# Kernel optimization log

Measured on AMD Instinct MI355X. Metric: run time of the kernel, lower is better.

Reference implementation:

```python
import jax, jax.numpy as jnp
from jax import lax
import numpy as np

DIM = 64
EMB = 48
PATCH = 8


def setup_inputs() -> dict:
    key = jax.random.key(0)
    ks = jax.random.split(key, 8)
    b, H, W = 4, 256, 256
    x = jax.random.normal(ks[0], (b, DIM, H, W), dtype=jnp.float32)
    prior = jax.random.normal(ks[1], (b, 1, EMB * 4), dtype=jnp.float32)
    # nn.Linear(embed_dim*4, dim*2, bias=False): weight [out, in]
    w_kernel = jax.random.normal(ks[2], (DIM * 2, EMB * 4), dtype=jnp.float32) * 0.05
    # Conv2d(dim, dim*6, 1)
    w_hidden = jax.random.normal(ks[3], (DIM * 6, DIM, 1, 1), dtype=jnp.float32) * 0.05
    # Conv2d(dim*6, dim*6, 3, padding=1, groups=dim*3) -> OIHW with I = 6*dim/(3*dim) = 2
    w_dw = jax.random.normal(ks[4], (DIM * 6, 2, 3, 3), dtype=jnp.float32) * 0.05
    # Conv2d(dim*2, dim, 1)
    w_proj = jax.random.normal(ks[5], (DIM, DIM * 2, 1, 1), dtype=jnp.float32) * 0.05
    ln_weight = jnp.ones((DIM * 2,), dtype=jnp.float32)
    ln_bias = jnp.zeros((DIM * 2,), dtype=jnp.float32)
    return {"x": x, "prior": prior, "w_kernel": w_kernel, "w_hidden": w_hidden,
            "w_dw": w_dw, "w_proj": w_proj, "ln_weight": ln_weight, "ln_bias": ln_bias}


def _patchify(t):
    # b c (h p1) (w p2) -> b c h w p1 p2
    b, c, H, W = t.shape
    t = t.reshape(b, c, H // PATCH, PATCH, W // PATCH, PATCH)
    return t.transpose(0, 1, 2, 4, 3, 5)


def _unpatchify(t):
    # b c h w p1 p2 -> b c (h p1) (w p2)
    b, c, h, w, p1, p2 = t.shape
    return t.transpose(0, 1, 2, 4, 3, 5).reshape(b, c, h * p1, w * p2)


def reference(x, prior, w_kernel, w_hidden, w_dw, w_proj, ln_weight, ln_bias):
    # prior modulation (group == 1 path)
    kv = jnp.einsum('blf,kf->blk', prior, w_kernel)[:, 0]  # [b, 2*dim]
    kv1 = kv[:, :DIM, None, None]
    kv2 = kv[:, DIM:, None, None]
    x = x * kv1 + kv2

    # 1x1 conv to hidden (6*dim channels)
    hidden = jnp.einsum('bchw,oc->bohw', x, w_hidden[:, :, 0, 0])

    # depthwise-ish 3x3 grouped conv, groups = 3*dim
    qkv = lax.conv_general_dilated(
        hidden, w_dw, window_strides=(1, 1), padding='SAME',
        feature_group_count=3 * DIM,
        dimension_numbers=('NCHW', 'OIHW', 'NCHW'))
    q, k, v = jnp.split(qkv, 3, axis=1)  # each [b, 2*dim, H, W]

    # frequency-domain correlation on 8x8 patches
    q_f = jnp.fft.rfft2(_patchify(q))
    k_f = jnp.fft.rfft2(_patchify(k))
    out = jnp.fft.irfft2(q_f * k_f, s=(PATCH, PATCH))
    out = _unpatchify(out)

    # WithBias LayerNorm over channel dim (to_3d puts channels last)
    mu = jnp.mean(out, axis=1, keepdims=True)
    var = jnp.mean((out - mu) ** 2, axis=1, keepdims=True)
    out = (out - mu) / jnp.sqrt(var + 1e-5)
    out = out * ln_weight[None, :, None, None] + ln_bias[None, :, None, None]

    # gate with v and project out
    output = v * out
    output = jnp.einsum('bchw,oc->bohw', output, w_proj[:, :, 0, 0])
    return output
```

## Files before the change

### kernel.cpp

```cpp
#include <hip/hip_runtime.h>


#define HW    65536
#define SLAB  64
#define HROWS 66
#define HSZ2  (HROWS*256)
#define QS    16384

__device__ __forceinline__ unsigned short f2bf(float f) {
    unsigned u = __float_as_uint(f);
    u += 0x7FFFu + ((u >> 16) & 1u);
    return (unsigned short)(u >> 16);
}
__device__ __forceinline__ float bflo(unsigned u) { return __uint_as_float(u << 16); }
__device__ __forceinline__ float bfhi(unsigned u) { return __uint_as_float(u & 0xFFFF0000u); }

__global__ void k_prep(const float* __restrict__ prior, const float* __restrict__ wk,
                       const float* __restrict__ wh, const float* __restrict__ wp,
                       float* __restrict__ kv, float* __restrict__ whT, float* __restrict__ wpT) {
    int t = blockIdx.x * 256 + threadIdx.x;
    if (t < 512) {
        int b = t >> 7, k = t & 127;
        const float* p = prior + b * 192;
        const float* w = wk + k * 192;
        float s = 0.f;
        for (int f = 0; f < 192; ++f) s = fmaf(p[f], w[f], s);
        kv[t] = s;
        return;
    }
    t -= 512;
    if (t < 24576) {
        int c = t / 384, o = t - c * 384;
        whT[t] = wh[o * 64 + c];
        return;
    }
    t -= 24576;
    int c = t >> 6, o = t & 63;
    wpT[t] = wp[o * 128 + c];
}

__global__ __launch_bounds__(256, 4) void k2_hidden(const float* __restrict__ x,
    const float* __restrict__ whT, const float* __restrict__ kv,
    unsigned short* __restrict__ hid, int r0) {
    int row = blockIdx.x * 2 + (threadIdx.x >> 7);
    int cp = threadIdx.x & 127;
    int chunk = blockIdx.y;
    int b = blockIdx.z;
    int g = r0 - 1 + row;
    unsigned* hb = (unsigned*)(hid + ((size_t)(b * 384 + chunk * 32)) * HSZ2
                               + row * 256 + cp * 2);
    if (g < 0 || g > 255) {
        #pragma unroll
        for (int j = 0; j < 32; ++j) hb[(size_t)j * (HSZ2 / 2)] = 0u;
        return;
    }
    const float2* xb = (const float2*)(x + (size_t)b * 64 * HW + g * 256 + cp * 2);
    const float* kv1 = kv + b * 128;
    const float* kv2 = kv1 + 64;
    float acc0[32], acc1[32];
    #pragma unroll
    for (int j = 0; j < 32; ++j) { acc0[j] = 0.f; acc1[j] = 0.f; }
    #pragma unroll 4
    for (int c = 0; c < 64; ++c) {
        float2 xv = xb[(size_t)c * (HW / 2)];
        float xp0 = fmaf(xv.x, kv1[c], kv2[c]);
        float xp1 = fmaf(xv.y, kv1[c], kv2[c]);
        const float* wr = whT + c * 384 + chunk * 32;
        #pragma unroll
        for (int j = 0; j < 32; ++j) {
            acc0[j] = fmaf(wr[j], xp0, acc0[j]);
            acc1[j] = fmaf(wr[j], xp1, acc1[j]);
        }
    }
    #pragma unroll
    for (int j = 0; j < 32; ++j)
        hb[(size_t)j * (HSZ2 / 2)] = (unsigned)f2bf(acc0[j]) | ((unsigned)f2bf(acc1[j]) << 16);
}

__global__ __launch_bounds__(256) void k3_dw(const unsigned short* __restrict__ hid,
    const float* __restrict__ wdw, unsigned short* __restrict__ qkv) {
    __shared__ float sIn[2 * 18 * 66];
    int t = threadIdx.x;
    int bid = blockIdx.x;
    int gl = blockIdx.y;
    int b = blockIdx.z;
    int tx = bid & 3, ty = bid >> 2;
    int x0 = tx * 64, y0 = ty * 16;
    const unsigned short* hbase = hid + ((size_t)(b * 384 + 2 * gl)) * HSZ2;
    for (int idx = t; idx < 2 * 18 * 66; idx += 256) {
        int chl = idx >= 1188;
        int rem = idx - chl * 1188;
        int row = rem / 66;
        int col = rem - row * 66;
        int gx = x0 + col - 1;
        float v = 0.f;
        if (gx >= 0 && gx < 256)
            v = bflo((unsigned)hbase[(size_t)chl * HSZ2 + (y0 + row) * 256 + gx]);
        sIn[idx] = v;
    }
    __syncthreads();
    int og = 2 * gl;
    float w0[18], w1[18];
    #pragma unroll
    for (int i = 0; i < 18; ++i) {
        w0[i] = wdw[(size_t)og * 18 + i];
        w1[i] = wdw[(size_t)(og + 1) * 18 + i];
    }
    unsigned short* q0 = qkv + ((size_t)(b * 384 + og)) * QS;
    #pragma unroll
    for (int pp = 0; pp < 2; ++pp) {
        int ly = pp * 8 + (t >> 5);
        int lxp = (t & 31) * 2;
        float a[2][2];
        #pragma unroll
        for (int px = 0; px < 2; ++px) {
            float s0 = 0.f, s1 = 0.f;
            #pragma unroll
            for (int i = 0; i < 2; ++i)
                #pragma unroll
                for (int ky = 0; ky < 3; ++ky)
                    #pragma unroll
                    for (int kx = 0; kx < 3; ++kx) {
                        float v = sIn[i * 1188 + (ly + ky) * 66 + (lxp + px + kx)];
                        s0 = fmaf(w0[i * 9 + ky * 3 + kx], v, s0);
                        s1 = fmaf(w1[i * 9 + ky * 3 + kx], v, s1);
                    }
            a[px][0] = s0; a[px][1] = s1;
        }
        int row = y0 + ly;
        int gx = x0 + lxp;
        int patch = (row >> 3) * 32 + (gx >> 3);
        int off = patch * 64 + (row & 7) * 8 + (gx & 7);
        ((unsigned*)(q0 + off))[0] =
            (unsigned)f2bf(a[0][0]) | ((unsigned)f2bf(a[1][0]) << 16);
        ((unsigned*)(q0 + QS + off))[0] =
            (unsigned)f2bf(a[0][1]) | ((unsigned)f2bf(a[1][1]) << 16);
    }
}

__global__ __launch_bounds__(256, 2) void kC_patch(const unsigned short* __restrict__ qkv,
    const float* __restrict__ wpT, const float* __restrict__ lnw,
    const float* __restrict__ lnb, float* __restrict__ outp, int r0) {
    __shared__ __align__(16) float sBuf[128 * 68];
    __shared__ __align__(16) float sMu[64];
    __shared__ __align__(16) float sRstd[64];
    int t = threadIdx.x;
    int p = blockIdx.x;
    int b = blockIdx.y;
    int c = t & 127;
    int pyh = t >> 7;

    const uint4* gq = (const uint4*)(qkv + ((size_t)(b * 384 + c)) * QS + p * 64);
    const uint4* gk = (const uint4*)(qkv + ((size_t)(b * 384 + 128 + c)) * QS + p * 64);
    float q[64], k[64];
    #pragma unroll
    for (int f = 0; f < 8; ++f) {
        uint4 u = gq[f];
        q[f * 8 + 0] = bflo(u.x); q[f * 8 + 1] = bfhi(u.x);
        q[f * 8 + 2] = bflo(u.y); q[f * 8 + 3] = bfhi(u.y);
        q[f * 8 + 4] = bflo(u.z); q[f * 8 + 5] = bfhi(u.z);
        q[f * 8 + 6] = bflo(u.w); q[f * 8 + 7] = bfhi(u.w);
    }
    #pragma unroll
    for (int s = 0; s < 8; ++s) {
        int r = (s + 4 * pyh) & 7;
        uint4 u = ((const uint4*)gk)[r];
        k[s * 8 + 0] = bflo(u.x); k[s * 8 + 1] = bfhi(u.x);
        k[s * 8 + 2] = bflo(u.y); k[s * 8 + 3] = bfhi(u.y);
        k[s * 8 + 4] = bflo(u.z); k[s * 8 + 5] = bfhi(u.z);
        k[s * 8 + 6] = bflo(u.w); k[s * 8 + 7] = bfhi(u.w);
    }
    float acc[4][8];
    #pragma unroll
    for (int it = 0; it < 4; ++it)
        #pragma unroll
        for (int px = 0; px < 8; ++px) acc[it][px] = 0.f;
    #pragma unroll
    for (int iy = 0; iy < 8; ++iy)
        #pragma unroll
        for (int ix = 0; ix < 8; ++ix) {
            float qv = q[iy * 8 + ix];
            #pragma unroll
            for (int it = 0; it < 4; ++it) {
                int ks = (it - iy) & 7;
                #pragma unroll
                for (int px = 0; px < 8; ++px)
                    acc[it][px] = fmaf(qv, k[ks * 8 + ((px - ix) & 7)], acc[it][px]);
            }
        }
    #pragma unroll
    for (int it = 0; it < 4; ++it) {
        int pix0 = pyh * 32 + it * 8;
        *(float4*)&sBuf[c * 68 + pix0] =
            make_float4(acc[it][0], acc[it][1], acc[it][2], acc[it][3]);
        *(float4*)&sBuf[c * 68 + pix0 + 4] =
            make_float4(acc[it][4], acc[it][5], acc[it][6], acc[it][7]);
    }
    const uint4* gv = (const uint4*)(qkv + ((size_t)(b * 384 + 256 + c)) * QS
                                     + p * 64 + pyh * 32);
    float vv[32];
    #pragma unroll
    for (int f = 0; f < 4; ++f) {
        uint4 u = gv[f];
        vv[f * 8 + 0] = bflo(u.x); vv[f * 8 + 1] = bfhi(u.x);
        vv[f * 8 + 2] = bflo(u.y); vv[f * 8 + 3] = bfhi(u.y);
        vv[f * 8 + 4] = bflo(u.z); vv[f * 8 + 5] = bfhi(u.z);
        vv[f * 8 + 6] = bflo(u.w); vv[f * 8 + 7] = bfhi(u.w);
    }
    float lw = lnw[c], lb = lnb[c];
    __syncthreads();

    {
        int q4 = (t >> 4) & 3;
        int px = (t & 15) | ((t >> 6) << 4);
        float s = 0.f, s2 = 0.f;
        #pragma unroll
        for (int j = 0; j < 32; ++j) {
            float v = sBuf[(q4 * 32 + j) * 68 + px];
            s += v;
            s2 = fmaf(v, v, s2);
        }
        s  += __shfl_xor(s, 16);   s2 += __shfl_xor(s2, 16);
        s  += __shfl_xor(s, 32);   s2 += __shfl_xor(s2, 32);
        if ((t & 48) == 0) {
            float mu = s * (1.f / 128.f);
            float var = s2 * (1.f / 128.f) - mu * mu;
            sMu[px] = mu;
            sRstd[px] = rsqrtf(var + 1e-5f);
        }
    }
    __syncthreads();
    #pragma unroll
    for (int it = 0; it < 4; ++it) {
        int pix0 = pyh * 32 + it * 8;
        float4 ma = *(const float4*)&sMu[pix0];
        float4 mb = *(const float4*)&sMu[pix0 + 4];
        float4 ra = *(const float4*)&sRstd[pix0];
        float4 rb = *(const float4*)&sRstd[pix0 + 4];
        float mus[8] = {ma.x, ma.y, ma.z, ma.w, mb.x, mb.y, mb.z, mb.w};
        float rss[8] = {ra.x, ra.y, ra.z, ra.w, rb.x, rb.y, rb.z, rb.w};
        #pragma unroll
        for (int px = 0; px < 8; ++px) {
            float tv = fmaf((acc[it][px] - mus[px]) * rss[px], lw, lb)
                       * vv[it * 8 + px];
            sBuf[(pix0 + px) * 132 + c] = tv;
        }
    }
    __syncthreads();
    {
        int px = t & 63;
        int og = __builtin_amdgcn_readfirstlane((t >> 6) * 16);
        float po[16];
        #pragma unroll
        for (int j = 0; j < 16; ++j) po[j] = 0.f;
        const float4* tb = (const float4*)&sBuf[px * 132];
        #pragma unroll 4
        for (int k4 = 0; k4 < 32; ++k4) {
            float4 tv = tb[k4];
            const float* w0 = wpT + (k4 * 4 + 0) * 64 + og;
            const float* w1 = wpT + (k4 * 4 + 1) * 64 + og;
            const float* w2 = wpT + (k4 * 4 + 2) * 64 + og;
            const float* w3 = wpT + (k4 * 4 + 3) * 64 + og;
            #pragma unroll
            for (int j = 0; j < 16; ++j)
                po[j] = fmaf(w0[j], tv.x,
                        fmaf(w1[j], tv.y,
                        fmaf(w2[j], tv.z,
                        fmaf(w3[j], tv.w, po[j]))));
        }
        int grow = r0 + (p >> 5) * 8 + (px >> 3);
        int gcol = (p & 31) * 8 + (px & 7);
        float* ob = outp + ((size_t)(b * 64 + og)) * HW + grow * 256 + gcol;
        #pragma unroll
        for (int j = 0; j < 16; ++j) ob[(size_t)j * HW] = po[j];
    }
}

extern "C" void kernel_launch(void* const* d_in, const int* in_sizes, int n_in,
                              void* d_out, int out_size, void* d_ws, size_t ws_size,
                              hipStream_t stream) {
    const float* x     = (const float*)d_in[0];
    const float* prior = (const float*)d_in[1];
    const float* wk    = (const float*)d_in[2];
    const float* wh    = (const float*)d_in[3];
    const float* wdw   = (const float*)d_in[4];
    const float* wp    = (const float*)d_in[5];
    const float* lnw   = (const float*)d_in[6];
    const float* lnb   = (const float*)d_in[7];
    float* out = (float*)d_out;
    float* ws  = (float*)d_ws;

    float* kv  = ws;
    float* whT = ws + 512;
    float* wpT = ws + 512 + 24576;
    unsigned short* hid = (unsigned short*)(ws + 40960);
    unsigned short* qkv = hid + (size_t)4 * 384 * HSZ2;

    k_prep<<<dim3(130), dim3(256), 0, stream>>>(prior, wk, wh, wp, kv, whT, wpT);
    for (int slab = 0; slab < 4; ++slab) {
        int r0 = slab * SLAB;
        k2_hidden<<<dim3(HROWS / 2, 12, 4), dim3(256), 0, stream>>>(x, whT, kv, hid, r0);
        k3_dw<<<dim3(16, 192, 4), dim3(256), 0, stream>>>(hid, wdw, qkv);
        kC_patch<<<dim3(256, 4), dim3(256), 0, stream>>>(qkv, wpT, lnw, lnb, out, r0);
    }
}
```

Before: 683.9 us.

## Restructure hidden 1x1 conv to load x once per pixel and loop output chunks

The hidden-projection kernel now assigns one pixel per thread and 192 output channels per block, instead of two pixels per thread and 32 channels per block. The 64 modulated input channels are loaded once into registers and reused across three 64-channel accumulator passes. This cuts redundant x reads, which before were repeated across 12 channel chunks. The cost is heavy register pressure (64 inputs plus 64 accumulators), a lower occupancy target, fewer blocks, and 16-bit stores instead of packed 32-bit stores.

```diff
diff --git a/kernel.cpp b/kernel.cpp
--- a/kernel.cpp
+++ b/kernel.cpp
@@ -39,42 +39,47 @@
     wpT[t] = wp[o * 128 + c];
 }
 
-__global__ __launch_bounds__(256, 4) void k2_hidden(const float* __restrict__ x,
+__global__ __launch_bounds__(256, 3) void k2_hidden(const float* __restrict__ x,
     const float* __restrict__ whT, const float* __restrict__ kv,
     unsigned short* __restrict__ hid, int r0) {
-    int row = blockIdx.x * 2 + (threadIdx.x >> 7);
-    int cp = threadIdx.x & 127;
-    int chunk = blockIdx.y;
+    int row = blockIdx.x;
+    int px  = threadIdx.x;
+    int half = blockIdx.y;
     int b = blockIdx.z;
     int g = r0 - 1 + row;
-    unsigned* hb = (unsigned*)(hid + ((size_t)(b * 384 + chunk * 32)) * HSZ2
-                               + row * 256 + cp * 2);
+    unsigned short* hb = hid + ((size_t)(b * 384 + half * 192)) * HSZ2
+                         + row * 256 + px;
     if (g < 0 || g > 255) {
-        #pragma unroll
-        for (int j = 0; j < 32; ++j) hb[(size_t)j * (HSZ2 / 2)] = 0u;
+        #pragma unroll 8
+        for (int j = 0; j < 192; ++j) hb[(size_t)j * HSZ2] = 0;
         return;
     }
-    const float2* xb = (const float2*)(x + (size_t)b * 64 * HW + g * 256 + cp * 2);
+    const float* xb = x + (size_t)b * 64 * HW + (size_t)g * 256 + px;
     const float* kv1 = kv + b * 128;
     const float* kv2 = kv1 + 64;
-    float acc0[32], acc1[32];
-    #pragma unroll
-    for (int j = 0; j < 32; ++j) { acc0[j] = 0.f; acc1[j] = 0.f; }
-    #pragma unroll 4
-    for (int c = 0; c < 64; ++c) {
-        float2 xv = xb[(size_t)c * (HW / 2)];
-        float xp0 = fmaf(xv.x, kv1[c], kv2[c]);
-        float xp1 = fmaf(xv.y, kv1[c], kv2[c]);
-        const float* wr = whT + c * 384 + chunk * 32;
-        #pragma unroll
-        for (int j = 0; j < 32; ++j) {
-            acc0[j] = fmaf(wr[j], xp0, acc0[j]);
-            acc1[j] = fmaf(wr[j], xp1, acc1[j]);
-        }
-    }
-    #pragma unroll
-    for (int j = 0; j < 32; ++j)
-        hb[(size_t)j * (HSZ2 / 2)] = (unsigned)f2bf(acc0[j]) | ((unsigned)f2bf(acc1[j]) << 16);
+    float xp[64];
+    #pragma unroll
+    for (int c = 0; c < 64; ++c)
+        xp[c] = fmaf(xb[(size_t)c * HW], kv1[c], kv2[c]);
+    #pragma unroll
+    for (int ch = 0; ch < 3; ++ch) {
+        const float* wbase = whT + half * 192 + ch * 64;
+        float acc[64];
+        #pragma unroll
+        for (int j = 0; j < 64; ++j) acc[j] = 0.f;
+        #pragma unroll 4
+        for (int c = 0; c < 64; ++c) {
+            float xv = xp[c];
+            const float* wr = wbase + c * 384;
+            #pragma unroll
+            for (int j = 0; j < 64; ++j)
+                acc[j] = fmaf(wr[j], xv, acc[j]);
+        }
+        unsigned short* hc = hb + (size_t)(ch * 64) * HSZ2;
+        #pragma unroll
+        for (int j = 0; j < 64; ++j)
+            hc[(size_t)j * HSZ2] = f2bf(acc[j]);
+    }
 }
 
 __global__ __launch_bounds__(256) void k3_dw(const unsigned short* __restrict__ hid,
@@ -299,7 +304,7 @@
     k_prep<<<dim3(130), dim3(256), 0, stream>>>(prior, wk, wh, wp, kv, whT, wpT);
     for (int slab = 0; slab < 4; ++slab) {
         int r0 = slab * SLAB;
-        k2_hidden<<<dim3(HROWS / 2, 12, 4), dim3(256), 0, stream>>>(x, whT, kv, hid, r0);
+        k2_hidden<<<dim3(HROWS, 2, 4), dim3(256), 0, stream>>>(x, whT, kv, hid, r0);
         k3_dw<<<dim3(16, 192, 4), dim3(256), 0, stream>>>(hid, wdw, qkv);
         kC_patch<<<dim3(256, 4), dim3(256), 0, stream>>>(qkv, wpT, lnw, lnb, out, r0);
     }
```

Result: slower. 751.7 us (+9.9%).
